# Kernel optimization log

Hardware: AMD Instinct MI355X
Metric: run time of the kernel (lower is better)

The kernel has to match this reference:

```python
import jax, jax.numpy as jnp
import numpy as np

N = 50000          # num nodes
E = 800000         # num directed edges
K = 10             # diffusion_iterations
ALPHA = 0.1        # teleportation_probability
D_IN, D_HID, N_CLS = 512, 128, 64


def _gcn_norm(edge_index, n):
    """Add self-loops and compute symmetric GCN normalization (PyG gcn_norm)."""
    loop = jnp.arange(n, dtype=edge_index.dtype)
    src = jnp.concatenate([edge_index[0], loop])  # message sources (x_j)
    dst = jnp.concatenate([edge_index[1], loop])  # aggregation targets
    deg = jax.ops.segment_sum(jnp.ones(src.shape[0], dtype=jnp.float32), dst,
                              num_segments=n)
    dinv = jnp.where(deg > 0, jax.lax.rsqrt(jnp.maximum(deg, 1.0)), 0.0)
    norm = dinv[src] * dinv[dst]  # [E+N]
    return src, dst, norm


def _appnp(x, src, dst, norm, n, k, alpha):
    """x_{t+1} = (1-alpha) * A_hat x_t + alpha * x_0, iterated k times."""
    h0 = x
    def step(xc, _):
        agg = jax.ops.segment_sum(xc[src] * norm[:, None], dst, num_segments=n)
        return (1.0 - alpha) * agg + alpha * h0, None
    xk, _ = jax.lax.scan(step, x, None, length=k)
    return xk


def setup_inputs() -> dict:
    key = jax.random.key(0)
    k1, k2, k3, k4 = jax.random.split(key, 4)
    x = jax.random.normal(k1, (N, D_IN), dtype=jnp.float32)
    edge_index = jax.random.randint(k2, (2, E), 0, N, dtype=jnp.int32)
    W1 = jax.random.normal(k3, (D_HID, D_IN), dtype=jnp.float32) / np.sqrt(D_IN)
    b1 = jnp.zeros((D_HID,), dtype=jnp.float32)
    W2 = jax.random.normal(k4, (N_CLS, D_HID), dtype=jnp.float32) / np.sqrt(D_HID)
    b2 = jnp.zeros((N_CLS,), dtype=jnp.float32)
    return {"x": x, "edge_index": edge_index, "W1": W1, "b1": b1,
            "W2": W2, "b2": b2}


def reference(x, edge_index, W1, b1, W2, b2):
    src, dst, norm = _gcn_norm(edge_index, N)
    # layer 0 (not last): linear + relu; since it is the second-to-last layer,
    # the recorded embedding is APPNP applied to its activation (x itself is
    # NOT replaced by the diffusion, matching the original forward).
    h1 = jax.nn.relu(x @ W1.T + b1)                    # [N, D_HID]
    emb1 = _appnp(h1, src, dst, norm, N, K, ALPHA)     # [N, D_HID]
    # last layer: linear only, then APPNP diffusion
    logits = h1 @ W2.T + b2                            # [N, N_CLS]
    out = _appnp(logits, src, dst, norm, N, K, ALPHA)  # [N, N_CLS]
    return (x, emb1, out)
```

## Files before the change

kernel.cpp:

```cpp
#include <hip/hip_runtime.h>

#define NN    50000
#define EE    800000
#define DIN   512
#define DH    128
#define NC    64
#define KITER 10
#define NSB   196
#define XSLB  6256

typedef __attribute__((ext_vector_type(8))) short short8;
typedef __attribute__((ext_vector_type(4))) short short4v;
typedef __attribute__((ext_vector_type(4))) float f32x4;

static __device__ __forceinline__ float bf2f(short u) {
  unsigned int x = ((unsigned int)(unsigned short)u) << 16;
  return __builtin_bit_cast(float, x);
}
static __device__ __forceinline__ short f2bf(float f) {
  unsigned int x = __builtin_bit_cast(unsigned int, f);
  unsigned int lsb = (x >> 16) & 1u;
  x += 0x7fffu + lsb;
  return (short)(x >> 16);
}

__global__ void k_copy_conv(const f32x4* __restrict__ src, f32x4* __restrict__ dst,
                            short4v* __restrict__ xb) {
  int i = blockIdx.x * 256 + threadIdx.x;
  f32x4 s = src[i];
  dst[i] = s;
  short4v o = { f2bf(s.x), f2bf(s.y), f2bf(s.z), f2bf(s.w) };
  xb[i] = o;
}

__global__ void k_copy4(const f32x4* __restrict__ src, f32x4* __restrict__ dst) {
  int i = blockIdx.x * 256 + threadIdx.x;
  dst[i] = src[i];
}

__global__ void k_f2bv(const float* __restrict__ src, short* __restrict__ dst) {
  int j = (blockIdx.x * 256 + threadIdx.x) * 4;
  f32x4 s = *(const f32x4*)(src + j);
  short4v o = { f2bf(s.x), f2bf(s.y), f2bf(s.z), f2bf(s.w) };
  *(short4v*)(dst + j) = o;
}

__global__ void k_count(const int* __restrict__ ei, int* __restrict__ cnt) {
  int e = blockIdx.x * 256 + threadIdx.x;
  if (e < EE) atomicAdd(&cnt[ei[EE + e]], 1);
}

__global__ __launch_bounds__(256) void k_scan1(const int* __restrict__ cnt,
                                               int* __restrict__ rp,
                                               int* __restrict__ bsum,
                                               float* __restrict__ dinv) {
  __shared__ int wsum[4];
  int t = threadIdx.x, lane = t & 63, w = t >> 6;
  int i = blockIdx.x * 256 + t;
  int x = (i < NN) ? cnt[i] : 0;
  if (i < NN) dinv[i] = rsqrtf((float)(x + 1));
  #pragma unroll
  for (int off = 1; off < 64; off <<= 1) {
    int y = __shfl_up(x, off);
    if (lane >= off) x += y;
  }
  if (lane == 63) wsum[w] = x;
  __syncthreads();
  int woff = 0;
  #pragma unroll
  for (int j = 0; j < 4; ++j) if (j < w) woff += wsum[j];
  x += woff;
  if (i < NN) rp[i + 1] = x;
  if (t == 255) bsum[blockIdx.x] = x;
}

__global__ __launch_bounds__(256) void k_scan2(int* __restrict__ bsum) {
  __shared__ int wsum[4];
  int t = threadIdx.x, lane = t & 63, w = t >> 6;
  int orig = (t < NSB) ? bsum[t] : 0;
  int x = orig;
  #pragma unroll
  for (int off = 1; off < 64; off <<= 1) {
    int y = __shfl_up(x, off);
    if (lane >= off) x += y;
  }
  if (lane == 63) wsum[w] = x;
  __syncthreads();
  int woff = 0;
  #pragma unroll
  for (int j = 0; j < 4; ++j) if (j < w) woff += wsum[j];
  x += woff;
  if (t < NSB) bsum[t] = x - orig;
}

__global__ __launch_bounds__(256) void k_scan3(int* __restrict__ rp,
                                               const int* __restrict__ bsum) {
  int i = blockIdx.x * 256 + threadIdx.x;
  if (i == 0) rp[0] = 0;
  if (i < NN) rp[i + 1] += bsum[blockIdx.x];
}

__global__ void k_fill(const int* __restrict__ ei, const int* __restrict__ rp,
                       int* __restrict__ fill, const float* __restrict__ dinv,
                       int* __restrict__ col, float* __restrict__ val) {
  int e = blockIdx.x * 256 + threadIdx.x;
  if (e < EE) {
    int s = ei[e], d = ei[EE + e];
    int pos = atomicAdd(&fill[d], 1);
    int idx = rp[d] + pos;
    col[idx] = s;
    val[idx] = dinv[s] * dinv[d];
  }
}

__global__ __launch_bounds__(256) void k_gemm1(const short* __restrict__ Xb,
                                               const short* __restrict__ W1b,
                                               const float* __restrict__ B1,
                                               short* __restrict__ h1s,
                                               float* __restrict__ st0) {
  int w = threadIdx.x >> 6;
  int lane = threadIdx.x & 63;
  int q = lane >> 4, r = lane & 15;
  int m0 = blockIdx.x * 64 + w * 16;

  f32x4 acc[8];
  #pragma unroll
  for (int i = 0; i < 8; ++i) acc[i] = (f32x4){0.f, 0.f, 0.f, 0.f};

  int row_a = m0 + r;
  if (row_a >= NN) row_a = NN - 1;
  const short* xrow = Xb + (size_t)row_a * DIN + q * 8;

  for (int kc = 0; kc < DIN / 32; ++kc) {
    short8 a = *(const short8*)(xrow + kc * 32);
    #pragma unroll
    for (int nt = 0; nt < 8; ++nt) {
      const short* wrow = W1b + (size_t)(nt * 16 + r) * DIN + q * 8 + kc * 32;
      short8 b = *(const short8*)wrow;
      acc[nt] = __builtin_amdgcn_mfma_f32_16x16x32_bf16(a, b, acc[nt], 0, 0, 0);
    }
  }

  #pragma unroll
  for (int nt = 0; nt < 8; ++nt) {
    float bias = B1[nt * 16 + r];
    #pragma unroll
    for (int reg = 0; reg < 4; ++reg) {
      int row = m0 + q * 4 + reg;
      if (row < NN) {
        float v = acc[nt][reg] + bias;
        v = v > 0.f ? v : 0.f;
        size_t sidx = (size_t)nt * NN * 16 + (size_t)row * 16 + r;
        h1s[sidx] = f2bf(v);
        st0[sidx] = v;
      }
    }
  }
}

__global__ __launch_bounds__(256) void k_step(const int* __restrict__ rp,
                                              const int* __restrict__ col,
                                              const float* __restrict__ val,
                                              const float* __restrict__ dinv,
                                              const float* __restrict__ xc,
                                              const short* __restrict__ h0,
                                              float* __restrict__ xn,
                                              const float* __restrict__ vc,
                                              float* __restrict__ vn,
                                              int first, int last) {
  if (blockIdx.x >= XSLB) {
    int i = (blockIdx.x - XSLB) * 256 + threadIdx.x;
    if (i >= NN) return;
    float s = 0.f;
    int e = rp[i], end = rp[i + 1];
    if (first) {
      for (; e + 4 <= end; e += 4) {
        float v0 = val[e], v1 = val[e+1], v2 = val[e+2], v3 = val[e+3];
        s += v0; s += v1; s += v2; s += v3;
      }
      for (; e < end; ++e) s += val[e];
      float di = dinv[i];
      s += di * di;
    } else {
      for (; e + 4 <= end; e += 4) {
        int c0 = col[e], c1 = col[e+1], c2 = col[e+2], c3 = col[e+3];
        float v0 = val[e]*vc[c0], v1 = val[e+1]*vc[c1];
        float v2 = val[e+2]*vc[c2], v3 = val[e+3]*vc[c3];
        s += v0; s += v1; s += v2; s += v3;
      }
      for (; e < end; ++e) s += val[e] * vc[col[e]];
      float di = dinv[i];
      s += di * di * vc[i];
    }
    vn[i] = 0.9f * s + 0.1f;
    return;
  }
  int sl = blockIdx.x & 7;
  int ck = blockIdx.x >> 3;
  int node = ck * 64 + (threadIdx.x >> 2);
  if (node >= NN) return;
  int fo = (threadIdx.x & 3) * 4;
  const float* xsl = xc + (size_t)sl * NN * 16;
  int e = rp[node], end = rp[node + 1];
  f32x4 xself = *(const f32x4*)(xsl + (size_t)node * 16 + fo);
  short4v hv  = *(const short4v*)(h0 + (size_t)sl * NN * 16 + (size_t)node * 16 + fo);
  float di = dinv[node];
  f32x4 acc = (f32x4){0.f, 0.f, 0.f, 0.f};
  for (; e + 4 <= end; e += 4) {
    int s0 = col[e], s1 = col[e+1], s2 = col[e+2], s3 = col[e+3];
    float w0 = val[e], w1 = val[e+1], w2 = val[e+2], w3 = val[e+3];
    f32x4 x0 = *(const f32x4*)(xsl + (size_t)s0 * 16 + fo);
    f32x4 x1 = *(const f32x4*)(xsl + (size_t)s1 * 16 + fo);
    f32x4 x2 = *(const f32x4*)(xsl + (size_t)s2 * 16 + fo);
    f32x4 x3 = *(const f32x4*)(xsl + (size_t)s3 * 16 + fo);
    acc += x0 * w0;
    acc += x1 * w1;
    acc += x2 * w2;
    acc += x3 * w3;
  }
  for (; e < end; ++e) {
    acc += *(const f32x4*)(xsl + (size_t)col[e] * 16 + fo) * val[e];
  }
  acc += xself * (di * di);
  f32x4 h = { bf2f(hv.x), bf2f(hv.y), bf2f(hv.z), bf2f(hv.w) };
  f32x4 res = acc * 0.9f + h * 0.1f;
  if (last) {
    *(f32x4*)(xn + (size_t)node * DH + sl * 16 + fo) = res;
  } else {
    *(f32x4*)(xn + (size_t)sl * NN * 16 + (size_t)node * 16 + fo) = res;
  }
}

__global__ __launch_bounds__(256) void k_gemm2(const float* __restrict__ emb,
                                               const float* __restrict__ W2,
                                               const float* __restrict__ B2,
                                               const float* __restrict__ v,
                                               float* __restrict__ out2) {
  __shared__ float sW[NC][DH + 1];
  __shared__ float sb[NC];
  __shared__ float sE[32][DH + 1];
  int t = threadIdx.x;
  for (int i = t; i < NC * DH; i += 256) sW[i / DH][i % DH] = W2[i];
  if (t < NC) sb[t] = B2[t];
  int n0 = blockIdx.x * 32;
  for (int i = t; i < 32 * DH; i += 256) {
    int nl = i / DH, kk = i % DH;
    int node = n0 + nl;
    sE[nl][kk] = (node < NN) ? emb[(size_t)node * DH + kk] : 0.f;
  }
  __syncthreads();
  int nl = t >> 3, cb = t & 7;
  int node = n0 + nl;
  if (node >= NN) return;
  float vn = v[node];
  #pragma unroll
  for (int j = 0; j < 8; ++j) {
    int c = cb + 8 * j;
    float s = 0.f;
    #pragma unroll 4
    for (int k = 0; k < DH; ++k) s += sE[nl][k] * sW[c][k];
    s += vn * sb[c];
    out2[(size_t)node * NC + c] = s;
  }
}

extern "C" void kernel_launch(void* const* d_in, const int* in_sizes, int n_in,
                              void* d_out, int out_size, void* d_ws, size_t ws_size,
                              hipStream_t stream) {
  const float* X  = (const float*)d_in[0];
  const int*   EI = (const int*)d_in[1];
  const float* W1 = (const float*)d_in[2];
  const float* B1 = (const float*)d_in[3];
  const float* W2 = (const float*)d_in[4];
  const float* B2 = (const float*)d_in[5];

  float* out0 = (float*)d_out;
  float* out1 = (float*)d_out + 25600000;
  float* out2 = (float*)d_out + 32000000;

  char* xr = (char*)d_in[0];
  const size_t XB_BYTES = (size_t)NN * DIN * sizeof(short);
  bool use_ws = (d_ws != nullptr) && (ws_size >= XB_BYTES);

  float* bufB = (float*)(xr);
  short* Xb   = use_ws ? (short*)d_ws : (short*)(xr);
  float* bufA = (float*)(xr + 51200000);
  short* h1   = (short*)(xr + 76800000);
  int*   col  = (int*)  (xr + 89600000);
  float* val  = (float*)(xr + 92800000);
  int*   rp   = (int*)  (xr + 96000000);
  int*   cnt  = (int*)  (xr + 96200192);
  int*   fill = (int*)  (xr + 96400192);
  float* dinv = (float*)(xr + 96600192);
  float* va   = (float*)(xr + 96800192);
  float* vb   = (float*)(xr + 97000192);
  short* W1b  = (short*)(xr + 97200192);
  int*   bsum = (int*)  (xr + 97400192);

  if (use_ws) {
    k_copy_conv<<<dim3(25000), dim3(256), 0, stream>>>(
        (const f32x4*)X, (f32x4*)out0, (short4v*)Xb);
  } else {
    k_copy4<<<dim3(25000), dim3(256), 0, stream>>>((const f32x4*)X, (f32x4*)out0);
    k_f2bv <<<dim3(25000), dim3(256), 0, stream>>>(out0, Xb);
  }
  k_f2bv <<<dim3(64), dim3(256), 0, stream>>>(W1, W1b);

  hipMemsetAsync(cnt, 0, 400000, stream);
  k_count<<<dim3(3125), dim3(256), 0, stream>>>(EI, cnt);
  k_scan1<<<dim3(NSB), dim3(256), 0, stream>>>(cnt, rp, bsum, dinv);
  k_scan2<<<dim3(1),   dim3(256), 0, stream>>>(bsum);
  k_scan3<<<dim3(NSB), dim3(256), 0, stream>>>(rp, bsum);
  k_fill <<<dim3(3125), dim3(256), 0, stream>>>(EI, rp, fill, dinv, col, val);

  k_gemm1<<<dim3(782), dim3(256), 0, stream>>>(Xb, W1b, B1, h1, bufA);

  for (int it = 0; it < KITER; ++it) {
    const float* xc = (it & 1) ? bufB : bufA;
    float*       xn = (it == KITER - 1) ? out1 : ((it & 1) ? bufA : bufB);
    const float* vcp = (it & 1) ? vb : va;
    float*       vnp = (it & 1) ? va : vb;
    k_step<<<dim3(XSLB + NSB), dim3(256), 0, stream>>>(
        rp, col, val, dinv, xc, h1, xn, vcp, vnp,
        it == 0 ? 1 : 0, it == KITER - 1 ? 1 : 0);
  }

  k_gemm2<<<dim3(1563), dim3(256), 0, stream>>>(out1, W2, B2, va, out2);
}
```

Baseline: 1.098 ms.

## Drop stored edge weights, recompute from dinv; unroll gather by 8 with nontemporal IO

After: 1.262 ms. 14.9% more time.

```diff
diff --git a/kernel.cpp b/kernel.cpp
--- a/kernel.cpp
+++ b/kernel.cpp
@@ -12,6 +12,7 @@
 typedef __attribute__((ext_vector_type(8))) short short8;
 typedef __attribute__((ext_vector_type(4))) short short4v;
 typedef __attribute__((ext_vector_type(4))) float f32x4;
+typedef unsigned long long ull;
 
 static __device__ __forceinline__ float bf2f(short u) {
   unsigned int x = ((unsigned int)(unsigned short)u) << 16;
@@ -101,15 +102,12 @@
 }
 
 __global__ void k_fill(const int* __restrict__ ei, const int* __restrict__ rp,
-                       int* __restrict__ fill, const float* __restrict__ dinv,
-                       int* __restrict__ col, float* __restrict__ val) {
+                       int* __restrict__ fill, int* __restrict__ col) {
   int e = blockIdx.x * 256 + threadIdx.x;
   if (e < EE) {
     int s = ei[e], d = ei[EE + e];
     int pos = atomicAdd(&fill[d], 1);
-    int idx = rp[d] + pos;
-    col[idx] = s;
-    val[idx] = dinv[s] * dinv[d];
+    col[rp[d] + pos] = s;
   }
 }
 
@@ -160,7 +158,6 @@
 
 __global__ __launch_bounds__(256) void k_step(const int* __restrict__ rp,
                                               const int* __restrict__ col,
-                                              const float* __restrict__ val,
                                               const float* __restrict__ dinv,
                                               const float* __restrict__ xc,
                                               const short* __restrict__ h0,
@@ -173,24 +170,25 @@
     if (i >= NN) return;
     float s = 0.f;
     int e = rp[i], end = rp[i + 1];
+    float dii = dinv[i];
     if (first) {
       for (; e + 4 <= end; e += 4) {
-        float v0 = val[e], v1 = val[e+1], v2 = val[e+2], v3 = val[e+3];
+        int c0 = col[e], c1 = col[e+1], c2 = col[e+2], c3 = col[e+3];
+        float v0 = dinv[c0] * dii, v1 = dinv[c1] * dii;
+        float v2 = dinv[c2] * dii, v3 = dinv[c3] * dii;
         s += v0; s += v1; s += v2; s += v3;
       }
-      for (; e < end; ++e) s += val[e];
-      float di = dinv[i];
-      s += di * di;
+      for (; e < end; ++e) s += dinv[col[e]] * dii;
+      s += dii * dii;
     } else {
       for (; e + 4 <= end; e += 4) {
         int c0 = col[e], c1 = col[e+1], c2 = col[e+2], c3 = col[e+3];
-        float v0 = val[e]*vc[c0], v1 = val[e+1]*vc[c1];
-        float v2 = val[e+2]*vc[c2], v3 = val[e+3]*vc[c3];
+        float v0 = (dinv[c0] * dii) * vc[c0], v1 = (dinv[c1] * dii) * vc[c1];
+        float v2 = (dinv[c2] * dii) * vc[c2], v3 = (dinv[c3] * dii) * vc[c3];
         s += v0; s += v1; s += v2; s += v3;
       }
-      for (; e < end; ++e) s += val[e] * vc[col[e]];
-      float di = dinv[i];
-      s += di * di * vc[i];
+      for (; e < end; ++e) s += (dinv[col[e]] * dii) * vc[col[e]];
+      s += dii * dii * vc[i];
     }
     vn[i] = 0.9f * s + 0.1f;
     return;
@@ -203,12 +201,38 @@
   const float* xsl = xc + (size_t)sl * NN * 16;
   int e = rp[node], end = rp[node + 1];
   f32x4 xself = *(const f32x4*)(xsl + (size_t)node * 16 + fo);
-  short4v hv  = *(const short4v*)(h0 + (size_t)sl * NN * 16 + (size_t)node * 16 + fo);
+  ull hq = __builtin_nontemporal_load(
+      (const ull*)(h0 + (size_t)sl * NN * 16 + (size_t)node * 16 + fo));
   float di = dinv[node];
   f32x4 acc = (f32x4){0.f, 0.f, 0.f, 0.f};
+  for (; e + 8 <= end; e += 8) {
+    int s0 = col[e],   s1 = col[e+1], s2 = col[e+2], s3 = col[e+3];
+    int s4 = col[e+4], s5 = col[e+5], s6 = col[e+6], s7 = col[e+7];
+    float w0 = dinv[s0] * di, w1 = dinv[s1] * di;
+    float w2 = dinv[s2] * di, w3 = dinv[s3] * di;
+    float w4 = dinv[s4] * di, w5 = dinv[s5] * di;
+    float w6 = dinv[s6] * di, w7 = dinv[s7] * di;
+    f32x4 x0 = *(const f32x4*)(xsl + (size_t)s0 * 16 + fo);
+    f32x4 x1 = *(const f32x4*)(xsl + (size_t)s1 * 16 + fo);
+    f32x4 x2 = *(const f32x4*)(xsl + (size_t)s2 * 16 + fo);
+    f32x4 x3 = *(const f32x4*)(xsl + (size_t)s3 * 16 + fo);
+    f32x4 x4 = *(const f32x4*)(xsl + (size_t)s4 * 16 + fo);
+    f32x4 x5 = *(const f32x4*)(xsl + (size_t)s5 * 16 + fo);
+    f32x4 x6 = *(const f32x4*)(xsl + (size_t)s6 * 16 + fo);
+    f32x4 x7 = *(const f32x4*)(xsl + (size_t)s7 * 16 + fo);
+    acc += x0 * w0;
+    acc += x1 * w1;
+    acc += x2 * w2;
+    acc += x3 * w3;
+    acc += x4 * w4;
+    acc += x5 * w5;
+    acc += x6 * w6;
+    acc += x7 * w7;
+  }
   for (; e + 4 <= end; e += 4) {
     int s0 = col[e], s1 = col[e+1], s2 = col[e+2], s3 = col[e+3];
-    float w0 = val[e], w1 = val[e+1], w2 = val[e+2], w3 = val[e+3];
+    float w0 = dinv[s0] * di, w1 = dinv[s1] * di;
+    float w2 = dinv[s2] * di, w3 = dinv[s3] * di;
     f32x4 x0 = *(const f32x4*)(xsl + (size_t)s0 * 16 + fo);
     f32x4 x1 = *(const f32x4*)(xsl + (size_t)s1 * 16 + fo);
     f32x4 x2 = *(const f32x4*)(xsl + (size_t)s2 * 16 + fo);
@@ -219,15 +243,17 @@
     acc += x3 * w3;
   }
   for (; e < end; ++e) {
-    acc += *(const f32x4*)(xsl + (size_t)col[e] * 16 + fo) * val[e];
+    int s = col[e];
+    acc += *(const f32x4*)(xsl + (size_t)s * 16 + fo) * (dinv[s] * di);
   }
   acc += xself * (di * di);
-  f32x4 h = { bf2f(hv.x), bf2f(hv.y), bf2f(hv.z), bf2f(hv.w) };
+  f32x4 h = { bf2f((short)hq), bf2f((short)(hq >> 16)),
+              bf2f((short)(hq >> 32)), bf2f((short)(hq >> 48)) };
   f32x4 res = acc * 0.9f + h * 0.1f;
   if (last) {
-    *(f32x4*)(xn + (size_t)node * DH + sl * 16 + fo) = res;
+    __builtin_nontemporal_store(res, (f32x4*)(xn + (size_t)node * DH + sl * 16 + fo));
   } else {
-    *(f32x4*)(xn + (size_t)sl * NN * 16 + (size_t)node * 16 + fo) = res;
+    __builtin_nontemporal_store(res, (f32x4*)(xn + (size_t)sl * NN * 16 + (size_t)node * 16 + fo));
   }
 }
 
@@ -287,7 +313,6 @@
   float* bufA = (float*)(xr + 51200000);
   short* h1   = (short*)(xr + 76800000);
   int*   col  = (int*)  (xr + 89600000);
-  float* val  = (float*)(xr + 92800000);
   int*   rp   = (int*)  (xr + 96000000);
   int*   cnt  = (int*)  (xr + 96200192);
   int*   fill = (int*)  (xr + 96400192);
@@ -311,7 +336,7 @@
   k_scan1<<<dim3(NSB), dim3(256), 0, stream>>>(cnt, rp, bsum, dinv);
   k_scan2<<<dim3(1),   dim3(256), 0, stream>>>(bsum);
   k_scan3<<<dim3(NSB), dim3(256), 0, stream>>>(rp, bsum);
-  k_fill <<<dim3(3125), dim3(256), 0, stream>>>(EI, rp, fill, dinv, col, val);
+  k_fill <<<dim3(3125), dim3(256), 0, stream>>>(EI, rp, fill, col);
 
   k_gemm1<<<dim3(782), dim3(256), 0, stream>>>(Xb, W1b, B1, h1, bufA);
 
@@ -321,7 +346,7 @@
     const float* vcp = (it & 1) ? vb : va;
     float*       vnp = (it & 1) ? va : vb;
     k_step<<<dim3(XSLB + NSB), dim3(256), 0, stream>>>(
-        rp, col, val, dinv, xc, h1, xn, vcp, vnp,
+        rp, col, dinv, xc, h1, xn, vcp, vnp,
         it == 0 ? 1 : 0, it == KITER - 1 ? 1 : 0);
   }
 
```
